# Kernel optimization log

Measured on AMD Instinct MI355X. Metric: run time of the kernel, lower is better.

The kernel has to match this reference:

```python
import jax, jax.numpy as jnp
import numpy as np
import math

ORDER = 4
FREQ = 160


def _layernorm(x, g, b, eps=1e-5):
    m = jnp.mean(x, axis=-1, keepdims=True)
    v = jnp.mean((x - m) ** 2, axis=-1, keepdims=True)
    return (x - m) / jnp.sqrt(v + eps) * g + b


def setup_inputs() -> dict:
    key = jax.random.key(0)
    ks = jax.random.split(key, 9)
    b, t, k, f = 8, 1000, ORDER, FREQ
    return {
        "far_complex": jax.random.normal(ks[0], (b, 2, f, t), jnp.float32),
        "mix_complex": jax.random.normal(ks[1], (b, 2, f, t), jnp.float32),
        "k_conv_w": jax.random.normal(ks[2], (2 * k, 2), jnp.float32) * 0.3,   # Conv2d(2 -> 2k, 1x1)
        "k_conv_b": jax.random.normal(ks[3], (2 * k,), jnp.float32) * 0.01,
        "ql_w": jax.random.normal(ks[4], (f, f), jnp.float32) / math.sqrt(f),  # query_linear
        "ql_b": jnp.zeros((f,), jnp.float32),
        "qn_g": jnp.ones((f,), jnp.float32),   # query_norm gamma
        "qn_b": jnp.zeros((f,), jnp.float32),  # query_norm beta
        "kl_w": jax.random.normal(ks[5], (k, k), jnp.float32) / math.sqrt(k),  # key_linear
        "kl_b": jnp.zeros((k,), jnp.float32),
        "kn_g": jnp.ones((k,), jnp.float32),
        "kn_b": jnp.zeros((k,), jnp.float32),
        "q_vec": jax.random.normal(ks[6], (f,), jnp.float32) * 0.5,  # query_vector
        "k_vec": jax.random.normal(ks[7], (k,), jnp.float32) * 0.5,  # key_vector
        "v_vec": jax.random.normal(ks[8], (k,), jnp.float32) * 0.5,  # value_vector
    }


def reference(far_complex, mix_complex, k_conv_w, k_conv_b, ql_w, ql_b,
              qn_g, qn_b, kl_w, kl_b, kn_g, kn_b, q_vec, k_vec, v_vec):
    b, c, f, t = far_complex.shape
    k = k_vec.shape[0]

    # im2col-style unfold over time with left padding (k-1)
    padded = jnp.pad(far_complex, ((0, 0), (0, 0), (0, 0), (k - 1, 0)))
    idx = jnp.arange(t)[:, None] + jnp.arange(k)[None, :]          # [t, k]
    unf = padded[..., idx]                                          # [b,2,f,t,k]
    unf_save = unf[:, 0] + 1j * unf[:, 1]                           # [b,f,t,k] complex64
    # in-place conjugation of imag channel (as in torch code)
    unf = jnp.stack([unf[:, 0], -unf[:, 1]], axis=1)                # [b,2,f,t,k]

    # per-channel outer products (torch does real matmul per channel)
    XTX = jnp.einsum('bcfti,bcftj->bcftij', unf, unf)               # [b,2,f,t,k,k]
    XTY = (unf * mix_complex[..., None])[..., None]                 # [b,2,f,t,k,1]

    query = jnp.transpose(unf, (0, 1, 3, 4, 2))                     # [b,2,t,k,f]
    kc = jnp.einsum('oc,bcft->boft', k_conv_w, mix_complex) + k_conv_b[None, :, None, None]
    key = jnp.transpose(kc.reshape(b, 2, k, f, t), (0, 1, 4, 3, 2))  # [b,2,t,f,k]

    value = jnp.swapaxes(jnp.concatenate([XTX, XTY], axis=-1), -1, -2)  # [b,2,f,t,k+1,k]

    query = _layernorm(query @ ql_w.T + ql_b, qn_g, qn_b) * jax.nn.sigmoid(q_vec)
    key = _layernorm(key @ kl_w.T + kl_b, kn_g, kn_b) * jax.nn.sigmoid(k_vec)
    value = value * jax.nn.sigmoid(v_vec)

    weight = jax.nn.softmax(query @ (key / math.sqrt(k)), axis=-1)  # [b,2,t,k,k]
    out = value @ weight[:, :, None]                                # [b,2,f,t,k+1,k]
    outT = jnp.swapaxes(out, -1, -2)                                # [b,2,f,t,k,k+1]
    XTX_new = outT[..., :k]                                         # [b,2,f,t,k,k]
    XTY_new = outT[..., k:]                                         # [b,2,f,t,k,1]
    XTX_c = XTX_new[:, 0] + 1j * XTX_new[:, 1]                      # [b,f,t,k,k]
    XTY_c = XTY_new[:, 0] + 1j * XTY_new[:, 1]                      # [b,f,t,k,1]

    eps = 1e-8
    eye_r = jnp.eye(k, dtype=jnp.float32) + eps
    eye = (eye_r + 1j * eye_r).astype(XTX_c.dtype)

    inv_XTX = jnp.linalg.inv(XTX_c + eye)                           # [b,f,t,k,k]
    wiener = (inv_XTX @ XTY_c)[..., 0]                              # [b,f,t,k]

    res = jnp.sum(unf_save * wiener, axis=-1)                       # [b,f,t]
    return jnp.stack([res.real, res.imag], axis=1)                  # [b,2,f,t]
```

## Files before the change

kernel.cpp:

```cpp
#include <hip/hip_runtime.h>
#include <math.h>

#define NBC   16
#define NF    160
#define NT    1000
#define NTP   1040

typedef __attribute__((ext_vector_type(8))) short short8;
typedef __attribute__((ext_vector_type(4))) float f32x4;

static __device__ __forceinline__ short f2bf(float x) {
    unsigned u = __builtin_bit_cast(unsigned, x);
    unsigned r = (u + 0x7fffu + ((u >> 16) & 1u)) >> 16;
    return (short)r;
}
static __device__ __forceinline__ float bf2f(short s) {
    unsigned u = ((unsigned)(unsigned short)s) << 16;
    return __builtin_bit_cast(float, u);
}

__global__ __launch_bounds__(640) void k1_mfma_ln(const float* __restrict__ far,
                                                  const float* __restrict__ qlw,
                                                  const float* __restrict__ qlb,
                                                  const float* __restrict__ qng,
                                                  const float* __restrict__ qnb,
                                                  const float* __restrict__ qvec,
                                                  float* __restrict__ Qn) {
    __shared__ float Xs[NF * 66];
    __shared__ short Bhi[5 * 4 * 64 * 8];
    __shared__ short Blo[5 * 4 * 64 * 8];
    __shared__ float redS[64 * 41];
    __shared__ float redQ[64 * 41];
    __shared__ float lnM[64], lnI[64];

    const int bc = blockIdx.x;
    const int t0 = blockIdx.y * 64;
    const int tid = threadIdx.x;
    const float sgn = (bc & 1) ? -1.f : 1.f;
    const float* Xb = far + (size_t)bc * NF * NT;

    const int w = __builtin_amdgcn_readfirstlane(tid >> 6);
    const int l = tid & 63;
    const int row = l & 15;
    const int kb = l >> 4;

    short8 Ahi[5], Alo[5];
    #pragma unroll
    for (int fc = 0; fc < 5; ++fc) {
        const float* ap = qlw + (size_t)(16 * w + row) * NF + fc * 32 + kb * 8;
        float4 x0 = *(const float4*)(ap + 0);
        float4 x1 = *(const float4*)(ap + 4);
        float xv[8] = {x0.x, x0.y, x0.z, x0.w, x1.x, x1.y, x1.z, x1.w};
        short8 h, lo;
        #pragma unroll
        for (int j = 0; j < 8; ++j) {
            short hj = f2bf(xv[j]);
            h[j] = hj;
            lo[j] = f2bf(xv[j] - bf2f(hj));
        }
        Ahi[fc] = h; Alo[fc] = lo;
    }

    #pragma unroll
    for (int i = 0; i < 16; ++i) {
        int o = tid + i * 640;
        int fi = o >> 6, tl0 = o & 63;
        int t = t0 + tl0;
        Xs[fi * 66 + tl0] = (t < NT) ? Xb[fi * NT + t] * sgn : 0.f;
    }
    __syncthreads();

    #pragma unroll
    for (int e = 0; e < 2; ++e) {
        int slot = tid * 2 + e;
        int sl = slot & 63;
        int g = slot >> 6;
        int fi0 = (g >> 2) * 32 + ((sl >> 4) << 3);
        int tloc = (g & 3) * 16 + (sl & 15);
        short8 h, lo;
        #pragma unroll
        for (int j = 0; j < 8; ++j) {
            float x = Xs[(fi0 + j) * 66 + tloc];
            short hj = f2bf(x);
            h[j] = hj;
            lo[j] = f2bf(x - bf2f(hj));
        }
        *(short8*)&Bhi[slot * 8] = h;
        *(short8*)&Blo[slot * 8] = lo;
    }
    __syncthreads();

    f32x4 acc0 = {0.f, 0.f, 0.f, 0.f}, acc1 = acc0, acc2 = acc0, acc3 = acc0;
    #pragma unroll
    for (int fc = 0; fc < 5; ++fc) {
        #pragma unroll
        for (int tt = 0; tt < 4; ++tt) {
            short8 bh = *(const short8*)&Bhi[((fc * 4 + tt) * 64 + l) * 8];
            short8 bl = *(const short8*)&Blo[((fc * 4 + tt) * 64 + l) * 8];
            f32x4 a = (tt == 0) ? acc0 : (tt == 1) ? acc1 : (tt == 2) ? acc2 : acc3;
            a = __builtin_amdgcn_mfma_f32_16x16x32_bf16(Ahi[fc], bh, a, 0, 0, 0);
            a = __builtin_amdgcn_mfma_f32_16x16x32_bf16(Ahi[fc], bl, a, 0, 0, 0);
            a = __builtin_amdgcn_mfma_f32_16x16x32_bf16(Alo[fc], bh, a, 0, 0, 0);
            if (tt == 0) acc0 = a; else if (tt == 1) acc1 = a; else if (tt == 2) acc2 = a; else acc3 = a;
        }
    }

    float qlbv[4], qngv[4], qnbv[4], sgqv[4];
    #pragma unroll
    for (int r = 0; r < 4; ++r) {
        int fo = 16 * w + kb * 4 + r;
        qlbv[r] = qlb[fo];
        qngv[r] = qng[fo];
        qnbv[r] = qnb[fo];
        sgqv[r] = 1.f / (1.f + expf(-qvec[fo]));
    }

    #pragma unroll
    for (int tt = 0; tt < 4; ++tt) {
        f32x4 a = (tt == 0) ? acc0 : (tt == 1) ? acc1 : (tt == 2) ? acc2 : acc3;
        float v0 = a[0] + qlbv[0], v1 = a[1] + qlbv[1];
        float v2 = a[2] + qlbv[2], v3 = a[3] + qlbv[3];
        float ps = v0 + v1 + v2 + v3;
        float pq = v0 * v0 + v1 * v1 + v2 * v2 + v3 * v3;
        int tl = tt * 16 + (l & 15);
        redS[tl * 41 + w * 4 + kb] = ps;
        redQ[tl * 41 + w * 4 + kb] = pq;
    }
    __syncthreads();

    if (tid < 64) {
        float s = 0.f, q = 0.f;
        #pragma unroll 8
        for (int j = 0; j < 40; ++j) {
            s += redS[tid * 41 + j];
            q += redQ[tid * 41 + j];
        }
        float mean = s * (1.f / NF);
        float var = q * (1.f / NF) - mean * mean;
        lnM[tid] = mean;
        lnI[tid] = 1.f / sqrtf(var + 1e-5f);
    }
    __syncthreads();

    float* Qb = Qn + (size_t)bc * NF * NTP;
    #pragma unroll
    for (int tt = 0; tt < 4; ++tt) {
        f32x4 a = (tt == 0) ? acc0 : (tt == 1) ? acc1 : (tt == 2) ? acc2 : acc3;
        int tl = tt * 16 + (l & 15);
        int t = t0 + tl;
        float mean = lnM[tl], inv = lnI[tl];
        if (t < NT) {
            #pragma unroll
            for (int r = 0; r < 4; ++r) {
                int fo = 16 * w + kb * 4 + r;
                float v = a[r] + qlbv[r];
                float vn = ((v - mean) * inv * qngv[r] + qnbv[r]) * sgqv[r];
                Qb[(size_t)fo * NTP + 3 + t] = vn;
            }
        }
    }

    if (t0 == 0 && tid < 3 * NF) {
        int ttp = tid / NF;
        int f = tid - ttp * NF;
        float s2 = 0.f, q2 = 0.f;
        for (int j = 0; j < NF; ++j) {
            float vj = qlb[j];
            s2 += vj;
            q2 = fmaf(vj, vj, q2);
        }
        float mn = s2 * (1.f / NF);
        float vr = q2 * (1.f / NF) - mn * mn;
        float iv = 1.f / sqrtf(vr + 1e-5f);
        float sq = 1.f / (1.f + expf(-qvec[f]));
        Qb[(size_t)f * NTP + ttp] = ((qlb[f] - mn) * iv * qng[f] + qnb[f]) * sq;
    }
}

__global__ __launch_bounds__(1024) void k3_attn_v4(const float* __restrict__ mix,
                                                   const float* __restrict__ Qn,
                                                   const float* __restrict__ kcw,
                                                   const float* __restrict__ kcb,
                                                   const float* __restrict__ klw,
                                                   const float* __restrict__ klb,
                                                   const float* __restrict__ kng,
                                                   const float* __restrict__ knb,
                                                   const float* __restrict__ kvec,
                                                   float* __restrict__ W) {
    __shared__ float buf[16 * 64 * 17];

    const int bc = blockIdx.x;
    const int t0 = blockIdx.y * 64;
    const int b = bc >> 1, c = bc & 1;
    const int tid = threadIdx.x;
    const int w = __builtin_amdgcn_readfirstlane(tid >> 6);
    const int lane = tid & 63;
    const int t = t0 + lane;
    const bool valid = t < NT;

    float kw0[4], kw1[4], kb[4], klwm[16], klbv[4], kngv[4], knbv[4], sigk[4];
    #pragma unroll
    for (int j = 0; j < 4; ++j) {
        kw0[j] = kcw[(4 * c + j) * 2 + 0];
        kw1[j] = kcw[(4 * c + j) * 2 + 1];
        kb[j]  = kcb[4 * c + j];
        klbv[j] = klb[j];
        kngv[j] = kng[j];
        knbv[j] = knb[j];
        sigk[j] = 0.5f / (1.f + expf(-kvec[j]));
    }
    #pragma unroll
    for (int x = 0; x < 16; ++x) klwm[x] = klw[x];

    float s[16];
    #pragma unroll
    for (int x = 0; x < 16; ++x) s[x] = 0.f;

    const float* mix0 = mix + (size_t)(b * 2) * NF * NT;
    const float* mix1 = mix0 + (size_t)NF * NT;
    const float* Qb = Qn + (size_t)bc * NF * NTP;
    const int f0 = w * 10;

    if (valid) {
        #pragma unroll 5
        for (int ff = 0; ff < 10; ++ff) {
            int f = f0 + ff;
            float m0 = mix0[(size_t)f * NT + t];
            float m1 = mix1[(size_t)f * NT + t];
            float kraw[4], klin[4];
            #pragma unroll
            for (int j = 0; j < 4; ++j)
                kraw[j] = fmaf(kw0[j], m0, fmaf(kw1[j], m1, kb[j]));
            #pragma unroll
            for (int jo = 0; jo < 4; ++jo) {
                float a = klbv[jo];
                #pragma unroll
                for (int ji = 0; ji < 4; ++ji) a = fmaf(klwm[jo * 4 + ji], kraw[ji], a);
                klin[jo] = a;
            }
            float mn = 0.25f * (klin[0] + klin[1] + klin[2] + klin[3]);
            float d0 = klin[0] - mn, d1 = klin[1] - mn, d2 = klin[2] - mn, d3 = klin[3] - mn;
            float var = 0.25f * (d0 * d0 + d1 * d1 + d2 * d2 + d3 * d3);
            float inv = 1.f / sqrtf(var + 1e-5f);
            float kn[4];
            kn[0] = (d0 * inv * kngv[0] + knbv[0]) * sigk[0];
            kn[1] = (d1 * inv * kngv[1] + knbv[1]) * sigk[1];
            kn[2] = (d2 * inv * kngv[2] + knbv[2]) * sigk[2];
            kn[3] = (d3 * inv * kngv[3] + knbv[3]) * sigk[3];

            const float* qp = Qb + (size_t)f * NTP + t;
            float q0 = qp[0], q1 = qp[1], q2 = qp[2], q3 = qp[3];
            #pragma unroll
            for (int j = 0; j < 4; ++j) {
                s[0 * 4 + j] = fmaf(q0, kn[j], s[0 * 4 + j]);
                s[1 * 4 + j] = fmaf(q1, kn[j], s[1 * 4 + j]);
                s[2 * 4 + j] = fmaf(q2, kn[j], s[2 * 4 + j]);
                s[3 * 4 + j] = fmaf(q3, kn[j], s[3 * 4 + j]);
            }
        }
    }

    {
        float* dst = &buf[(w * 64 + lane) * 17];
        #pragma unroll
        for (int q4 = 0; q4 < 4; ++q4) {
            float4 v = {s[q4 * 4 + 0], s[q4 * 4 + 1], s[q4 * 4 + 2], s[q4 * 4 + 3]};
            *(float4*)(dst + q4 * 4) = v;
        }
    }
    __syncthreads();

    if (tid < 256) {
        int q4 = tid >> 6;
        int ln = tid & 63;
        int tt = t0 + ln;
        if (tt < NT) {
            float4 a = *(const float4*)&buf[(0 * 64 + ln) * 17 + q4 * 4];
            #pragma unroll
            for (int ww = 1; ww < 16; ++ww) {
                float4 p = *(const float4*)&buf[(ww * 64 + ln) * 17 + q4 * 4];
                a.x += p.x; a.y += p.y; a.z += p.z; a.w += p.w;
            }
            float mx = fmaxf(fmaxf(a.x, a.y), fmaxf(a.z, a.w));
            float e0 = expf(a.x - mx), e1 = expf(a.y - mx);
            float e2 = expf(a.z - mx), e3 = expf(a.w - mx);
            float inv = 1.f / (e0 + e1 + e2 + e3);
            float4 v = {e0 * inv, e1 * inv, e2 * inv, e3 * inv};
            *(float4*)(W + ((size_t)bc * NT + tt) * 16 + q4 * 4) = v;
        }
    }
}

__device__ __forceinline__ void csolve4(float Ar[16], float Ai[16],
                                        float br[4], float bi[4],
                                        float wr[4], float wi[4]) {
    #pragma unroll
    for (int col = 0; col < 4; ++col) {
        #pragma unroll
        for (int r = col + 1; r < 4; ++r) {
            float cp = fabsf(Ar[col * 4 + col]) + fabsf(Ai[col * 4 + col]);
            float cr = fabsf(Ar[r * 4 + col]) + fabsf(Ai[r * 4 + col]);
            bool sw = cr > cp;
            #pragma unroll
            for (int m = col; m < 4; ++m) {
                float a0 = Ar[col * 4 + m], a1 = Ar[r * 4 + m];
                Ar[col * 4 + m] = sw ? a1 : a0;
                Ar[r * 4 + m]   = sw ? a0 : a1;
                float c0 = Ai[col * 4 + m], c1 = Ai[r * 4 + m];
                Ai[col * 4 + m] = sw ? c1 : c0;
                Ai[r * 4 + m]   = sw ? c0 : c1;
            }
            float b0 = br[col], b1 = br[r];
            br[col] = sw ? b1 : b0; br[r] = sw ? b0 : b1;
            float d0 = bi[col], d1 = bi[r];
            bi[col] = sw ? d1 : d0; bi[r] = sw ? d0 : d1;
        }
        float pr = Ar[col * 4 + col], pi = Ai[col * 4 + col];
        float den = 1.f / (pr * pr + pi * pi);
        #pragma unroll
        for (int r = col + 1; r < 4; ++r) {
            float nr = Ar[r * 4 + col], ni = Ai[r * 4 + col];
            float fr = (nr * pr + ni * pi) * den;
            float fi = (ni * pr - nr * pi) * den;
            #pragma unroll
            for (int m = col + 1; m < 4; ++m) {
                float tr = Ar[col * 4 + m], ti = Ai[col * 4 + m];
                Ar[r * 4 + m] -= fr * tr - fi * ti;
                Ai[r * 4 + m] -= fr * ti + fi * tr;
            }
            float tr = br[col], ti = bi[col];
            br[r] -= fr * tr - fi * ti;
            bi[r] -= fr * ti + fi * tr;
        }
    }
    #pragma unroll
    for (int col = 3; col >= 0; --col) {
        float sr = br[col], si = bi[col];
        #pragma unroll
        for (int m = col + 1; m < 4; ++m) {
            float tr = Ar[col * 4 + m], ti = Ai[col * 4 + m];
            sr -= tr * wr[m] - ti * wi[m];
            si -= tr * wi[m] + ti * wr[m];
        }
        float pr = Ar[col * 4 + col], pi = Ai[col * 4 + col];
        float den = 1.f / (pr * pr + pi * pi);
        wr[col] = (sr * pr + si * pi) * den;
        wi[col] = (si * pr - sr * pi) * den;
    }
}

__global__ __launch_bounds__(256) void k4_final(const float* __restrict__ far,
                                                const float* __restrict__ mix,
                                                const float* __restrict__ Wt,
                                                const float* __restrict__ vvec,
                                                float* __restrict__ out) {
    const int t = blockIdx.x * 256 + threadIdx.x;
    const int f = blockIdx.y;
    const int b = blockIdx.z;
    if (t >= NT) return;

    const float* fr  = far + (size_t)(b * 2 + 0) * NF * NT + (size_t)f * NT;
    const float* fim = far + (size_t)(b * 2 + 1) * NF * NT + (size_t)f * NT;
    float ur[4], ui[4];
    #pragma unroll
    for (int d = 0; d < 4; ++d) {
        int tp = t - 3 + d;
        bool ok = tp >= 0;
        ur[d] = ok ? fr[tp] : 0.f;
        ui[d] = ok ? fim[tp] : 0.f;
    }
    float m0 = mix[(size_t)(b * 2 + 0) * NF * NT + (size_t)f * NT + t];
    float m1 = mix[(size_t)(b * 2 + 1) * NF * NT + (size_t)f * NT + t];

    float sv[4];
    #pragma unroll
    for (int i = 0; i < 4; ++i) sv[i] = 1.f / (1.f + expf(-vvec[i]));

    const float* w0p = Wt + ((size_t)(b * 2 + 0) * NT + t) * 16;
    const float* w1p = Wt + ((size_t)(b * 2 + 1) * NT + t) * 16;

    float g0[4], g1[4];
    #pragma unroll
    for (int j = 0; j < 4; ++j) { g0[j] = 0.f; g1[j] = 0.f; }
    #pragma unroll
    for (int i = 0; i < 4; ++i) {
        float a0 = ur[i] * sv[i];
        float a1 = -ui[i] * sv[i];
        #pragma unroll
        for (int j = 0; j < 4; ++j) {
            g0[j] = fmaf(a0, w0p[i * 4 + j], g0[j]);
            g1[j] = fmaf(a1, w1p[i * 4 + j], g1[j]);
        }
    }

    float Ar[16], Ai[16], br[4], bi[4], wr[4], wi[4];
    #pragma unroll
    for (int j = 0; j < 4; ++j) {
        #pragma unroll
        for (int m = 0; m < 4; ++m) {
            float e = (j == m) ? (1.0f + 1e-8f) : 1e-8f;
            Ar[j * 4 + m] = fmaf(ur[m], g0[j], e);
            Ai[j * 4 + m] = fmaf(-ui[m], g1[j], e);
        }
        br[j] = m0 * g0[j];
        bi[j] = m1 * g1[j];
    }

    csolve4(Ar, Ai, br, bi, wr, wi);

    float resr = 0.f, resi = 0.f;
    #pragma unroll
    for (int d = 0; d < 4; ++d) {
        resr += ur[d] * wr[d] - ui[d] * wi[d];
        resi += ur[d] * wi[d] + ui[d] * wr[d];
    }
    out[(size_t)(b * 2 + 0) * NF * NT + (size_t)f * NT + t] = resr;
    out[(size_t)(b * 2 + 1) * NF * NT + (size_t)f * NT + t] = resi;
}

extern "C" void kernel_launch(void* const* d_in, const int* in_sizes, int n_in,
                              void* d_out, int out_size, void* d_ws, size_t ws_size,
                              hipStream_t stream) {
    const float* far  = (const float*)d_in[0];
    const float* mix  = (const float*)d_in[1];
    const float* kcw  = (const float*)d_in[2];
    const float* kcb  = (const float*)d_in[3];
    const float* qlw  = (const float*)d_in[4];
    const float* qlb  = (const float*)d_in[5];
    const float* qng  = (const float*)d_in[6];
    const float* qnb  = (const float*)d_in[7];
    const float* klw  = (const float*)d_in[8];
    const float* klb  = (const float*)d_in[9];
    const float* kng  = (const float*)d_in[10];
    const float* knb  = (const float*)d_in[11];
    const float* qvec = (const float*)d_in[12];
    const float* kvec = (const float*)d_in[13];
    const float* vvec = (const float*)d_in[14];

    float* Qn = (float*)d_ws;
    float* W  = Qn + (size_t)NBC * NF * NTP;
    float* out = (float*)d_out;

    k1_mfma_ln<<<dim3(NBC, 16), 640, 0, stream>>>(far, qlw, qlb, qng, qnb, qvec, Qn);
    k3_attn_v4<<<dim3(NBC, 16), 1024, 0, stream>>>(mix, Qn, kcw, kcb, klw, klb,
                                                   kng, knb, kvec, W);
    k4_final<<<dim3(4, NF, 8), 256, 0, stream>>>(far, mix, W, vvec, out);
}
```

Baseline: 57.00 us.

## Fuse query linear/layernorm kernel into attention kernel via LDS with halo recompute

Merges the query projection and layernorm kernel into the attention-weight kernel. Each block recomputes the three-step left halo by processing 80 time columns instead of 64, and the normalized query tile stays in shared memory, so the global Qn workspace round trip and one kernel launch go away. The cost is about 25% redundant MFMA work for the halo, a larger LDS footprint (~155KB per block) that limits residency, and 6 of 16 waves sitting idle during the matmul phase.

```diff
diff --git a/kernel.cpp b/kernel.cpp
--- a/kernel.cpp
+++ b/kernel.cpp
@@ -4,7 +4,6 @@
 #define NBC   16
 #define NF    160
 #define NT    1000
-#define NTP   1040
 
 typedef __attribute__((ext_vector_type(8))) short short8;
 typedef __attribute__((ext_vector_type(4))) float f32x4;
@@ -19,116 +18,135 @@
     return __builtin_bit_cast(float, u);
 }
 
-__global__ __launch_bounds__(640) void k1_mfma_ln(const float* __restrict__ far,
-                                                  const float* __restrict__ qlw,
-                                                  const float* __restrict__ qlb,
-                                                  const float* __restrict__ qng,
-                                                  const float* __restrict__ qnb,
-                                                  const float* __restrict__ qvec,
-                                                  float* __restrict__ Qn) {
-    __shared__ float Xs[NF * 66];
-    __shared__ short Bhi[5 * 4 * 64 * 8];
-    __shared__ short Blo[5 * 4 * 64 * 8];
-    __shared__ float redS[64 * 41];
-    __shared__ float redQ[64 * 41];
-    __shared__ float lnM[64], lnI[64];
+__global__ __launch_bounds__(1024, 4) void k13_fused(const float* __restrict__ far,
+                                                     const float* __restrict__ mix,
+                                                     const float* __restrict__ qlw,
+                                                     const float* __restrict__ qlb,
+                                                     const float* __restrict__ qng,
+                                                     const float* __restrict__ qnb,
+                                                     const float* __restrict__ qvec,
+                                                     const float* __restrict__ kcw,
+                                                     const float* __restrict__ kcb,
+                                                     const float* __restrict__ klw,
+                                                     const float* __restrict__ klb,
+                                                     const float* __restrict__ kng,
+                                                     const float* __restrict__ knb,
+                                                     const float* __restrict__ kvec,
+                                                     float* __restrict__ W) {
+    __shared__ float pool[38720];
+    __shared__ float lnM[80], lnI[80];
+    float* Qlds = pool;
+    float* Xs   = pool + 12960;
+    short* Bhi  = (short*)(pool + 25920);
+    short* Blo  = (short*)(pool + 32320);
+    float* redS = Xs;
+    float* redQ = Xs + 3280;
+    float* sbuf = Xs;
 
     const int bc = blockIdx.x;
     const int t0 = blockIdx.y * 64;
     const int tid = threadIdx.x;
-    const float sgn = (bc & 1) ? -1.f : 1.f;
-    const float* Xb = far + (size_t)bc * NF * NT;
-
     const int w = __builtin_amdgcn_readfirstlane(tid >> 6);
     const int l = tid & 63;
+    const int b = bc >> 1, c = bc & 1;
+    const float sgn = c ? -1.f : 1.f;
+    const float* Xb = far + (size_t)bc * NF * NT;
+
     const int row = l & 15;
     const int kb = l >> 4;
 
     short8 Ahi[5], Alo[5];
-    #pragma unroll
-    for (int fc = 0; fc < 5; ++fc) {
-        const float* ap = qlw + (size_t)(16 * w + row) * NF + fc * 32 + kb * 8;
-        float4 x0 = *(const float4*)(ap + 0);
-        float4 x1 = *(const float4*)(ap + 4);
-        float xv[8] = {x0.x, x0.y, x0.z, x0.w, x1.x, x1.y, x1.z, x1.w};
-        short8 h, lo;
-        #pragma unroll
-        for (int j = 0; j < 8; ++j) {
-            short hj = f2bf(xv[j]);
-            h[j] = hj;
-            lo[j] = f2bf(xv[j] - bf2f(hj));
-        }
-        Ahi[fc] = h; Alo[fc] = lo;
-    }
-
-    #pragma unroll
-    for (int i = 0; i < 16; ++i) {
-        int o = tid + i * 640;
-        int fi = o >> 6, tl0 = o & 63;
-        int t = t0 + tl0;
-        Xs[fi * 66 + tl0] = (t < NT) ? Xb[fi * NT + t] * sgn : 0.f;
+    if (w < 10) {
+        #pragma unroll
+        for (int fc = 0; fc < 5; ++fc) {
+            const float* ap = qlw + (size_t)(16 * w + row) * NF + fc * 32 + kb * 8;
+            float4 x0 = *(const float4*)(ap + 0);
+            float4 x1 = *(const float4*)(ap + 4);
+            float xv[8] = {x0.x, x0.y, x0.z, x0.w, x1.x, x1.y, x1.z, x1.w};
+            short8 h, lo;
+            #pragma unroll
+            for (int j = 0; j < 8; ++j) {
+                short hj = f2bf(xv[j]);
+                h[j] = hj;
+                lo[j] = f2bf(xv[j] - bf2f(hj));
+            }
+            Ahi[fc] = h; Alo[fc] = lo;
+        }
+    }
+
+    #pragma unroll
+    for (int i = 0; i < 13; ++i) {
+        int o = tid + i * 1024;
+        if (o < 12800) {
+            int fi = o / 80, j = o - fi * 80;
+            int tq = t0 - 3 + j;
+            float v = (tq >= 0 && tq < NT) ? Xb[fi * NT + tq] * sgn : 0.f;
+            Xs[fi * 81 + j] = v;
+        }
     }
     __syncthreads();
 
     #pragma unroll
     for (int e = 0; e < 2; ++e) {
-        int slot = tid * 2 + e;
-        int sl = slot & 63;
-        int g = slot >> 6;
-        int fi0 = (g >> 2) * 32 + ((sl >> 4) << 3);
-        int tloc = (g & 3) * 16 + (sl & 15);
-        short8 h, lo;
-        #pragma unroll
-        for (int j = 0; j < 8; ++j) {
-            float x = Xs[(fi0 + j) * 66 + tloc];
-            short hj = f2bf(x);
-            h[j] = hj;
-            lo[j] = f2bf(x - bf2f(hj));
-        }
-        *(short8*)&Bhi[slot * 8] = h;
-        *(short8*)&Blo[slot * 8] = lo;
-    }
-    __syncthreads();
-
-    f32x4 acc0 = {0.f, 0.f, 0.f, 0.f}, acc1 = acc0, acc2 = acc0, acc3 = acc0;
-    #pragma unroll
-    for (int fc = 0; fc < 5; ++fc) {
-        #pragma unroll
-        for (int tt = 0; tt < 4; ++tt) {
-            short8 bh = *(const short8*)&Bhi[((fc * 4 + tt) * 64 + l) * 8];
-            short8 bl = *(const short8*)&Blo[((fc * 4 + tt) * 64 + l) * 8];
-            f32x4 a = (tt == 0) ? acc0 : (tt == 1) ? acc1 : (tt == 2) ? acc2 : acc3;
-            a = __builtin_amdgcn_mfma_f32_16x16x32_bf16(Ahi[fc], bh, a, 0, 0, 0);
-            a = __builtin_amdgcn_mfma_f32_16x16x32_bf16(Ahi[fc], bl, a, 0, 0, 0);
-            a = __builtin_amdgcn_mfma_f32_16x16x32_bf16(Alo[fc], bh, a, 0, 0, 0);
-            if (tt == 0) acc0 = a; else if (tt == 1) acc1 = a; else if (tt == 2) acc2 = a; else acc3 = a;
-        }
-    }
-
-    float qlbv[4], qngv[4], qnbv[4], sgqv[4];
-    #pragma unroll
-    for (int r = 0; r < 4; ++r) {
-        int fo = 16 * w + kb * 4 + r;
-        qlbv[r] = qlb[fo];
-        qngv[r] = qng[fo];
-        qnbv[r] = qnb[fo];
-        sgqv[r] = 1.f / (1.f + expf(-qvec[fo]));
-    }
-
-    #pragma unroll
-    for (int tt = 0; tt < 4; ++tt) {
-        f32x4 a = (tt == 0) ? acc0 : (tt == 1) ? acc1 : (tt == 2) ? acc2 : acc3;
-        float v0 = a[0] + qlbv[0], v1 = a[1] + qlbv[1];
-        float v2 = a[2] + qlbv[2], v3 = a[3] + qlbv[3];
-        float ps = v0 + v1 + v2 + v3;
-        float pq = v0 * v0 + v1 * v1 + v2 * v2 + v3 * v3;
-        int tl = tt * 16 + (l & 15);
-        redS[tl * 41 + w * 4 + kb] = ps;
-        redQ[tl * 41 + w * 4 + kb] = pq;
-    }
-    __syncthreads();
-
-    if (tid < 64) {
+        int tk = tid + e * 1024;
+        if (tk < 1600) {
+            int g = tk >> 6;
+            int sl = tk & 63;
+            int tt = g / 5, fc = g - 5 * tt;
+            int fi0 = fc * 32 + ((sl >> 4) << 3);
+            int j0 = tt * 16 + (sl & 15);
+            short8 h, lo;
+            #pragma unroll
+            for (int j = 0; j < 8; ++j) {
+                float x = Xs[(fi0 + j) * 81 + j0];
+                short hj = f2bf(x);
+                h[j] = hj;
+                lo[j] = f2bf(x - bf2f(hj));
+            }
+            *(short8*)&Bhi[tk * 8] = h;
+            *(short8*)&Blo[tk * 8] = lo;
+        }
+    }
+    __syncthreads();
+
+    f32x4 acc0 = {0.f, 0.f, 0.f, 0.f}, acc1 = acc0, acc2 = acc0, acc3 = acc0, acc4 = acc0;
+    float qlbv[4], gam[4], bet[4];
+    if (w < 10) {
+        #pragma unroll
+        for (int fc = 0; fc < 5; ++fc) {
+            #pragma unroll
+            for (int tt = 0; tt < 5; ++tt) {
+                short8 bh = *(const short8*)&Bhi[((tt * 5 + fc) * 64 + l) * 8];
+                short8 bl = *(const short8*)&Blo[((tt * 5 + fc) * 64 + l) * 8];
+                f32x4 a = (tt == 0) ? acc0 : (tt == 1) ? acc1 : (tt == 2) ? acc2 : (tt == 3) ? acc3 : acc4;
+                a = __builtin_amdgcn_mfma_f32_16x16x32_bf16(Ahi[fc], bh, a, 0, 0, 0);
+                a = __builtin_amdgcn_mfma_f32_16x16x32_bf16(Ahi[fc], bl, a, 0, 0, 0);
+                a = __builtin_amdgcn_mfma_f32_16x16x32_bf16(Alo[fc], bh, a, 0, 0, 0);
+                if (tt == 0) acc0 = a; else if (tt == 1) acc1 = a; else if (tt == 2) acc2 = a;
+                else if (tt == 3) acc3 = a; else acc4 = a;
+            }
+        }
+        #pragma unroll
+        for (int r = 0; r < 4; ++r) {
+            int fo = 16 * w + kb * 4 + r;
+            qlbv[r] = qlb[fo];
+            float sq = 1.f / (1.f + expf(-qvec[fo]));
+            gam[r] = qng[fo] * sq;
+            bet[r] = qnb[fo] * sq;
+        }
+        #pragma unroll
+        for (int tt = 0; tt < 5; ++tt) {
+            f32x4 a = (tt == 0) ? acc0 : (tt == 1) ? acc1 : (tt == 2) ? acc2 : (tt == 3) ? acc3 : acc4;
+            float v0 = a[0] + qlbv[0], v1 = a[1] + qlbv[1];
+            float v2 = a[2] + qlbv[2], v3 = a[3] + qlbv[3];
+            int j = tt * 16 + row;
+            redS[j * 41 + w * 4 + kb] = v0 + v1 + v2 + v3;
+            redQ[j * 41 + w * 4 + kb] = v0 * v0 + v1 * v1 + v2 * v2 + v3 * v3;
+        }
+    }
+    __syncthreads();
+
+    if (tid < 80) {
         float s = 0.f, q = 0.f;
         #pragma unroll 8
         for (int j = 0; j < 40; ++j) {
@@ -142,68 +160,28 @@
     }
     __syncthreads();
 
-    float* Qb = Qn + (size_t)bc * NF * NTP;
-    #pragma unroll
-    for (int tt = 0; tt < 4; ++tt) {
-        f32x4 a = (tt == 0) ? acc0 : (tt == 1) ? acc1 : (tt == 2) ? acc2 : acc3;
-        int tl = tt * 16 + (l & 15);
-        int t = t0 + tl;
-        float mean = lnM[tl], inv = lnI[tl];
-        if (t < NT) {
+    if (w < 10) {
+        #pragma unroll
+        for (int tt = 0; tt < 5; ++tt) {
+            f32x4 a = (tt == 0) ? acc0 : (tt == 1) ? acc1 : (tt == 2) ? acc2 : (tt == 3) ? acc3 : acc4;
+            int j = tt * 16 + row;
+            float mean = lnM[j], inv = lnI[j];
             #pragma unroll
             for (int r = 0; r < 4; ++r) {
                 int fo = 16 * w + kb * 4 + r;
                 float v = a[r] + qlbv[r];
-                float vn = ((v - mean) * inv * qngv[r] + qnbv[r]) * sgqv[r];
-                Qb[(size_t)fo * NTP + 3 + t] = vn;
-            }
-        }
-    }
-
-    if (t0 == 0 && tid < 3 * NF) {
-        int ttp = tid / NF;
-        int f = tid - ttp * NF;
-        float s2 = 0.f, q2 = 0.f;
-        for (int j = 0; j < NF; ++j) {
-            float vj = qlb[j];
-            s2 += vj;
-            q2 = fmaf(vj, vj, q2);
-        }
-        float mn = s2 * (1.f / NF);
-        float vr = q2 * (1.f / NF) - mn * mn;
-        float iv = 1.f / sqrtf(vr + 1e-5f);
-        float sq = 1.f / (1.f + expf(-qvec[f]));
-        Qb[(size_t)f * NTP + ttp] = ((qlb[f] - mn) * iv * qng[f] + qnb[f]) * sq;
-    }
-}
-
-__global__ __launch_bounds__(1024) void k3_attn_v4(const float* __restrict__ mix,
-                                                   const float* __restrict__ Qn,
-                                                   const float* __restrict__ kcw,
-                                                   const float* __restrict__ kcb,
-                                                   const float* __restrict__ klw,
-                                                   const float* __restrict__ klb,
-                                                   const float* __restrict__ kng,
-                                                   const float* __restrict__ knb,
-                                                   const float* __restrict__ kvec,
-                                                   float* __restrict__ W) {
-    __shared__ float buf[16 * 64 * 17];
-
-    const int bc = blockIdx.x;
-    const int t0 = blockIdx.y * 64;
-    const int b = bc >> 1, c = bc & 1;
-    const int tid = threadIdx.x;
-    const int w = __builtin_amdgcn_readfirstlane(tid >> 6);
-    const int lane = tid & 63;
-    const int t = t0 + lane;
-    const bool valid = t < NT;
-
-    float kw0[4], kw1[4], kb[4], klwm[16], klbv[4], kngv[4], knbv[4], sigk[4];
+                Qlds[fo * 81 + j] = (v - mean) * inv * gam[r] + bet[r];
+            }
+        }
+    }
+    __syncthreads();
+
+    float kw0[4], kw1[4], kbv[4], klwm[16], klbv[4], kngv[4], knbv[4], sigk[4];
     #pragma unroll
     for (int j = 0; j < 4; ++j) {
         kw0[j] = kcw[(4 * c + j) * 2 + 0];
         kw1[j] = kcw[(4 * c + j) * 2 + 1];
-        kb[j]  = kcb[4 * c + j];
+        kbv[j] = kcb[4 * c + j];
         klbv[j] = klb[j];
         kngv[j] = kng[j];
         knbv[j] = knb[j];
@@ -212,17 +190,20 @@
     #pragma unroll
     for (int x = 0; x < 16; ++x) klwm[x] = klw[x];
 
+    const int ts = l;
+    const int t = t0 + ts;
+    const bool valid = t < NT;
+
     float s[16];
     #pragma unroll
     for (int x = 0; x < 16; ++x) s[x] = 0.f;
 
     const float* mix0 = mix + (size_t)(b * 2) * NF * NT;
     const float* mix1 = mix0 + (size_t)NF * NT;
-    const float* Qb = Qn + (size_t)bc * NF * NTP;
     const int f0 = w * 10;
 
     if (valid) {
-        #pragma unroll 5
+        #pragma unroll
         for (int ff = 0; ff < 10; ++ff) {
             int f = f0 + ff;
             float m0 = mix0[(size_t)f * NT + t];
@@ -230,7 +211,7 @@
             float kraw[4], klin[4];
             #pragma unroll
             for (int j = 0; j < 4; ++j)
-                kraw[j] = fmaf(kw0[j], m0, fmaf(kw1[j], m1, kb[j]));
+                kraw[j] = fmaf(kw0[j], m0, fmaf(kw1[j], m1, kbv[j]));
             #pragma unroll
             for (int jo = 0; jo < 4; ++jo) {
                 float a = klbv[jo];
@@ -248,8 +229,10 @@
             kn[2] = (d2 * inv * kngv[2] + knbv[2]) * sigk[2];
             kn[3] = (d3 * inv * kngv[3] + knbv[3]) * sigk[3];
 
-            const float* qp = Qb + (size_t)f * NTP + t;
-            float q0 = qp[0], q1 = qp[1], q2 = qp[2], q3 = qp[3];
+            float q0 = Qlds[f * 81 + ts + 0];
+            float q1 = Qlds[f * 81 + ts + 1];
+            float q2 = Qlds[f * 81 + ts + 2];
+            float q3 = Qlds[f * 81 + ts + 3];
             #pragma unroll
             for (int j = 0; j < 4; ++j) {
                 s[0 * 4 + j] = fmaf(q0, kn[j], s[0 * 4 + j]);
@@ -261,7 +244,7 @@
     }
 
     {
-        float* dst = &buf[(w * 64 + lane) * 17];
+        float* dst = &sbuf[(w * 64 + l) * 17];
         #pragma unroll
         for (int q4 = 0; q4 < 4; ++q4) {
             float4 v = {s[q4 * 4 + 0], s[q4 * 4 + 1], s[q4 * 4 + 2], s[q4 * 4 + 3]};
@@ -275,10 +258,10 @@
         int ln = tid & 63;
         int tt = t0 + ln;
         if (tt < NT) {
-            float4 a = *(const float4*)&buf[(0 * 64 + ln) * 17 + q4 * 4];
+            float4 a = *(const float4*)&sbuf[(0 * 64 + ln) * 17 + q4 * 4];
             #pragma unroll
             for (int ww = 1; ww < 16; ++ww) {
-                float4 p = *(const float4*)&buf[(ww * 64 + ln) * 17 + q4 * 4];
+                float4 p = *(const float4*)&sbuf[(ww * 64 + ln) * 17 + q4 * 4];
                 a.x += p.x; a.y += p.y; a.z += p.z; a.w += p.w;
             }
             float mx = fmaxf(fmaxf(a.x, a.y), fmaxf(a.z, a.w));
@@ -437,12 +420,10 @@
     const float* kvec = (const float*)d_in[13];
     const float* vvec = (const float*)d_in[14];
 
-    float* Qn = (float*)d_ws;
-    float* W  = Qn + (size_t)NBC * NF * NTP;
+    float* W = (float*)d_ws;
     float* out = (float*)d_out;
 
-    k1_mfma_ln<<<dim3(NBC, 16), 640, 0, stream>>>(far, qlw, qlb, qng, qnb, qvec, Qn);
-    k3_attn_v4<<<dim3(NBC, 16), 1024, 0, stream>>>(mix, Qn, kcw, kcb, klw, klb,
-                                                   kng, knb, kvec, W);
+    k13_fused<<<dim3(NBC, 16), 1024, 0, stream>>>(far, mix, qlw, qlb, qng, qnb, qvec,
+                                                  kcw, kcb, klw, klb, kng, knb, kvec, W);
     k4_final<<<dim3(4, NF, 8), 256, 0, stream>>>(far, mix, W, vvec, out);
 }
```

After: 52.06 us. 8.7% less time.
